# Kernel tuning notes

Measured on AMD Instinct MI355X. Metric: run time of the kernel, lower is better.

## Reference

```python
import jax, jax.numpy as jnp
import numpy as np

BATCH, N_STEPS, STATE_DIM = 8192, 128, 16
HIDDEN = 50
IN0 = STATE_DIM + 1  # features + prev_delta


def _lstm_cell(x, h, c, w_ih, w_hh, b):
    # PyTorch gate order: i, f, g, o
    gates = x @ w_ih.T + h @ w_hh.T + b  # (B, 4H)
    i, f, g, o = jnp.split(gates, 4, axis=-1)
    c_new = jax.nn.sigmoid(f) * c + jax.nn.sigmoid(i) * jnp.tanh(g)
    h_new = jax.nn.sigmoid(o) * jnp.tanh(c_new)
    return h_new, c_new


def setup_inputs() -> dict:
    key = jax.random.key(0)
    ks = jax.random.split(key, 8)
    s = 0.1
    return {
        "features": jax.random.normal(ks[0], (BATCH, N_STEPS, STATE_DIM), dtype=jnp.float32),
        "w_ih0": jax.random.normal(ks[1], (4 * HIDDEN, IN0), dtype=jnp.float32) * s,
        "w_hh0": jax.random.normal(ks[2], (4 * HIDDEN, HIDDEN), dtype=jnp.float32) * s,
        "b_0": jnp.zeros((4 * HIDDEN,), dtype=jnp.float32),  # bias_ih + bias_hh (both init to 0)
        "w_ih1": jax.random.normal(ks[3], (4 * HIDDEN, HIDDEN), dtype=jnp.float32) * s,
        "w_hh1": jax.random.normal(ks[4], (4 * HIDDEN, HIDDEN), dtype=jnp.float32) * s,
        "b_1": jnp.zeros((4 * HIDDEN,), dtype=jnp.float32),
        "w_fc1": jax.random.normal(ks[5], (HIDDEN // 2, HIDDEN), dtype=jnp.float32) * s,
        "b_fc1": jnp.zeros((HIDDEN // 2,), dtype=jnp.float32),
        "w_fc2": jax.random.normal(ks[6], (1, HIDDEN // 2), dtype=jnp.float32) * s,
        "b_fc2": jnp.zeros((1,), dtype=jnp.float32),
    }


def reference(features, w_ih0, w_hh0, b_0, w_ih1, w_hh1, b_1, w_fc1, b_fc1, w_fc2, b_fc2):
    B = features.shape[0]
    feats_t = jnp.swapaxes(features, 0, 1)  # (T, B, state_dim)
    z = jnp.zeros((B, HIDDEN), dtype=features.dtype)
    init = (z, z, z, z, jnp.zeros((B, 1), dtype=features.dtype))

    def step(carry, x_t):
        h0, c0, h1, c1, prev_delta = carry
        x = jnp.concatenate([x_t, prev_delta], axis=-1)  # (B, state_dim+1)
        h0, c0 = _lstm_cell(x, h0, c0, w_ih0, w_hh0, b_0)
        h1, c1 = _lstm_cell(h0, h1, c1, w_ih1, w_hh1, b_1)
        delta = jax.nn.relu(h1 @ w_fc1.T + b_fc1) @ w_fc2.T + b_fc2  # (B, 1)
        return (h0, c0, h1, c1, delta), delta[:, 0]

    _, deltas = jax.lax.scan(step, init, feats_t)  # (T, B)
    return jnp.swapaxes(deltas, 0, 1)  # (B, T)
```

## Files before the change

kernel.cpp:

```cpp
#include <hip/hip_runtime.h>
#include <math.h>

#define BATCH    8192
#define TSTEPS   128
#define SDIM     16
#define HID      50
#define IN0      17
#define BT       16
#define NTHREADS 256

#define RS      160
#define OFF_H0  32
#define OFF_H1  96
#define W0K     96
#define W1K     128
#define WFK     64

typedef _Float16 half_t;
typedef __attribute__((ext_vector_type(8))) _Float16 half8;
typedef __attribute__((ext_vector_type(4))) float    floatx4;

#define MFMA16(a, b, c) __builtin_amdgcn_mfma_f32_16x16x32_f16((a), (b), (c), 0, 0, 0)

__device__ __forceinline__ float sig_u(float x) {
    float e = __expf(-x);
    return __builtin_amdgcn_rcpf(1.0f + e);
}
__device__ __forceinline__ float tanh_u(float x) {
    float e = __expf(-2.0f * x);
    return fmaf(2.0f, __builtin_amdgcn_rcpf(1.0f + e), -1.0f);
}
__device__ __forceinline__ void hsplit(float v, half_t* hp, half_t* lp) {
    half_t h = (half_t)v;
    *hp = h;
    *lp = (half_t)(v - (float)h);
}

__global__ __launch_bounds__(NTHREADS, 2)
void lstm2_uni_kernel(const float* __restrict__ feat,
                      const float* __restrict__ w_ih0,
                      const float* __restrict__ w_hh0,
                      const float* __restrict__ b_0,
                      const float* __restrict__ w_ih1,
                      const float* __restrict__ w_hh1,
                      const float* __restrict__ b_1,
                      const float* __restrict__ w_fc1,
                      const float* __restrict__ b_fc1,
                      const float* __restrict__ w_fc2,
                      const float* __restrict__ b_fc2,
                      float* __restrict__ out)
{
    __shared__ __align__(16) half_t smW[128 * W1K];
    __shared__ __align__(16) half_t Xh[2][BT * RS];
    __shared__ __align__(16) half_t Xl[2][BT * RS];

    const int tid  = threadIdx.x;
    const int lane = tid & 63;
    const int wv   = tid >> 6;
    const int quad = lane >> 4;
    const int col  = lane & 15;
    const int k0q  = quad * 8;
    const int b0   = blockIdx.x * BT;

    auto w0val = [&](int r, int k) -> float {
        if (r >= 200) return 0.0f;
        int j = r >> 2, q = r & 3, orig = q * HID + j;
        if (k < IN0) return w_ih0[orig * IN0 + k];
        if (k < OFF_H0) return 0.0f;
        int u = k - OFF_H0;
        return (u < HID) ? w_hh0[orig * HID + u] : 0.0f;
    };
    auto w1val = [&](int r, int k) -> float {
        if (r >= 200) return 0.0f;
        int j = r >> 2, q = r & 3, orig = q * HID + j;
        if (k < 64) { return (k < HID) ? w_ih1[orig * HID + k] : 0.0f; }
        int u = k - 64;
        return (u < HID) ? w_hh1[orig * HID + u] : 0.0f;
    };

    const int lrow = 64 * (wv & 1) + col;
    half8 a0f[3][4], a1f[4][4];

    #pragma unroll 1
    for (int h = 0; h < 2; ++h) {
        for (int i = tid; i < 128 * W0K; i += NTHREADS) {
            int r = i / W0K, kk = i - r * W0K;
            smW[i] = (half_t)w0val(128 * h + r, kk);
        }
        __syncthreads();
        if ((wv >> 1) == h) {
            #pragma unroll
            for (int kt = 0; kt < 3; ++kt)
                #pragma unroll
                for (int ti = 0; ti < 4; ++ti)
                    a0f[kt][ti] = *(const half8*)(smW + (lrow + 16 * ti) * W0K + 32 * kt + k0q);
        }
        __syncthreads();
    }
    #pragma unroll 1
    for (int h = 0; h < 2; ++h) {
        for (int i = tid; i < 128 * W1K; i += NTHREADS) {
            int r = i >> 7, kk = i & 127;
            smW[i] = (half_t)w1val(128 * h + r, kk);
        }
        __syncthreads();
        if ((wv >> 1) == h) {
            #pragma unroll
            for (int kt = 0; kt < 4; ++kt)
                #pragma unroll
                for (int ti = 0; ti < 4; ++ti)
                    a1f[kt][ti] = *(const half8*)(smW + (lrow + 16 * ti) * W1K + 32 * kt + k0q);
        }
        __syncthreads();
    }
    for (int i = tid; i < 32 * WFK; i += NTHREADS) {
        int r = i >> 6, kk = i & 63;
        smW[i] = (half_t)((r < 25 && kk < HID) ? w_fc1[r * HID + kk] : 0.0f);
    }
    for (int i = tid; i < BT * RS; i += NTHREADS) {
        Xh[0][i] = (half_t)0.0f; Xl[0][i] = (half_t)0.0f;
        Xh[1][i] = (half_t)0.0f; Xl[1][i] = (half_t)0.0f;
    }
    __syncthreads();

    const half8 hz = {0, 0, 0, 0, 0, 0, 0, 0};
    half8 wff[2][2];
    wff[0][0] = hz; wff[0][1] = hz; wff[1][0] = hz; wff[1][1] = hz;
    if (wv == 0) {
        #pragma unroll
        for (int kt = 0; kt < 2; ++kt)
            #pragma unroll
            for (int tf = 0; tf < 2; ++tf)
                wff[kt][tf] = *(const half8*)(smW + (16 * tf + col) * WFK + 32 * kt + k0q);
    }

    const int xs = tid >> 4, xk = tid & 15;
    const size_t fbase = (size_t)(b0 + xs) * (TSTEPS * SDIM) + xk;
    hsplit(feat[fbase], &Xh[0][xs * RS + xk], &Xl[0][xs * RS + xk]);

    floatx4 bias0[4], bias1[4];
    #pragma unroll
    for (int ti = 0; ti < 4; ++ti) {
        floatx4 z = {0.f, 0.f, 0.f, 0.f};
        bias0[ti] = z; bias1[ti] = z;
        int u = 4 * (4 * wv + ti) + quad;
        if (u < HID) {
            bias0[ti][0] = b_0[u];           bias0[ti][1] = b_0[HID + u];
            bias0[ti][2] = b_0[2 * HID + u]; bias0[ti][3] = b_0[3 * HID + u];
            bias1[ti][0] = b_1[u];           bias1[ti][1] = b_1[HID + u];
            bias1[ti][2] = b_1[2 * HID + u]; bias1[ti][3] = b_1[3 * HID + u];
        }
    }
    floatx4 w2r[2], bfr[2];
    { floatx4 z = {0.f, 0.f, 0.f, 0.f}; w2r[0] = z; w2r[1] = z; bfr[0] = z; bfr[1] = z; }
    float bf2 = 0.0f;
    if (wv == 0) {
        bf2 = b_fc2[0];
        #pragma unroll
        for (int tf = 0; tf < 2; ++tf)
            #pragma unroll
            for (int r5 = 0; r5 < 4; ++r5) {
                int r = 16 * tf + quad * 4 + r5;
                if (r < 25) { w2r[tf][r5] = w_fc2[r]; bfr[tf][r5] = b_fc1[r]; }
            }
    }

    float c0s[4] = {0.f, 0.f, 0.f, 0.f};
    float c1s[4] = {0.f, 0.f, 0.f, 0.f};
    half8 nb1h = hz, nb1l = hz, nb2h = hz, nb2l = hz;

    half_t* Xhc = Xh[0]; half_t* Xlc = Xl[0];
    half_t* Xhn = Xh[1]; half_t* Xln = Xl[1];
    __syncthreads();

    for (int t = 0; t < TSTEPS; ++t) {
        float fnext = (t + 1 < TSTEPS) ? feat[fbase + (size_t)(t + 1) * SDIM] : 0.0f;

        floatx4 acc[4];
        #pragma unroll
        for (int ti = 0; ti < 4; ++ti) acc[ti] = bias0[ti];
        {
            half8 bh = *(const half8*)(Xhc + col * RS + k0q);
            half8 bl = *(const half8*)(Xlc + col * RS + k0q);
            #pragma unroll
            for (int ti = 0; ti < 4; ++ti) {
                acc[ti] = MFMA16(a0f[0][ti], bh, acc[ti]);
                acc[ti] = MFMA16(a0f[0][ti], bl, acc[ti]);
            }
        }
        #pragma unroll
        for (int ti = 0; ti < 4; ++ti) {
            acc[ti] = MFMA16(a0f[1][ti], nb1h, acc[ti]);
            acc[ti] = MFMA16(a0f[1][ti], nb1l, acc[ti]);
            acc[ti] = MFMA16(a0f[2][ti], nb2h, acc[ti]);
            acc[ti] = MFMA16(a0f[2][ti], nb2l, acc[ti]);
        }

        #pragma unroll
        for (int ti = 0; ti < 4; ++ti) {
            int u = 4 * (4 * wv + ti) + quad;
            float i_ = sig_u(acc[ti][0]);
            float f_ = sig_u(acc[ti][1]);
            float g_ = tanh_u(acc[ti][2]);
            float o_ = sig_u(acc[ti][3]);
            float c  = f_ * c0s[ti] + i_ * g_;
            c0s[ti]  = c;
            float hv = o_ * tanh_u(c);
            half_t hh, hl; hsplit(hv, &hh, &hl);
            Xhn[col * RS + OFF_H0 + u] = hh;
            Xln[col * RS + OFF_H0 + u] = hl;
        }
        __syncthreads();

        floatx4 acc1[4];
        #pragma unroll
        for (int ti = 0; ti < 4; ++ti) acc1[ti] = bias1[ti];
        nb1h = *(const half8*)(Xhn + col * RS + OFF_H0 + k0q);
        nb1l = *(const half8*)(Xln + col * RS + OFF_H0 + k0q);
        #pragma unroll
        for (int ti = 0; ti < 4; ++ti) {
            acc1[ti] = MFMA16(a1f[0][ti], nb1h, acc1[ti]);
            acc1[ti] = MFMA16(a1f[0][ti], nb1l, acc1[ti]);
        }
        nb2h = *(const half8*)(Xhn + col * RS + OFF_H0 + 32 + k0q);
        nb2l = *(const half8*)(Xln + col * RS + OFF_H0 + 32 + k0q);
        #pragma unroll
        for (int ti = 0; ti < 4; ++ti) {
            acc1[ti] = MFMA16(a1f[1][ti], nb2h, acc1[ti]);
            acc1[ti] = MFMA16(a1f[1][ti], nb2l, acc1[ti]);
        }
        #pragma unroll
        for (int kt = 2; kt < 4; ++kt) {
            half8 bh = *(const half8*)(Xhc + col * RS + OFF_H1 + 32 * (kt - 2) + k0q);
            half8 bl = *(const half8*)(Xlc + col * RS + OFF_H1 + 32 * (kt - 2) + k0q);
            #pragma unroll
            for (int ti = 0; ti < 4; ++ti) {
                acc1[ti] = MFMA16(a1f[kt][ti], bh, acc1[ti]);
                acc1[ti] = MFMA16(a1f[kt][ti], bl, acc1[ti]);
            }
        }

        #pragma unroll
        for (int ti = 0; ti < 4; ++ti) {
            int u = 4 * (4 * wv + ti) + quad;
            float i_ = sig_u(acc1[ti][0]);
            float f_ = sig_u(acc1[ti][1]);
            float g_ = tanh_u(acc1[ti][2]);
            float o_ = sig_u(acc1[ti][3]);
            float c  = f_ * c1s[ti] + i_ * g_;
            c1s[ti]  = c;
            float hv = o_ * tanh_u(c);
            half_t hh, hl; hsplit(hv, &hh, &hl);
            Xhn[col * RS + OFF_H1 + u] = hh;
            Xln[col * RS + OFF_H1 + u] = hl;
        }
        __syncthreads();

        if (wv == 0) {
            floatx4 accf[2]; accf[0] = bfr[0]; accf[1] = bfr[1];
            #pragma unroll
            for (int kt = 0; kt < 2; ++kt) {
                half8 bh = *(const half8*)(Xhn + col * RS + OFF_H1 + 32 * kt + k0q);
                half8 bl = *(const half8*)(Xln + col * RS + OFF_H1 + 32 * kt + k0q);
                #pragma unroll
                for (int tf = 0; tf < 2; ++tf) {
                    accf[tf] = MFMA16(wff[kt][tf], bh, accf[tf]);
                    accf[tf] = MFMA16(wff[kt][tf], bl, accf[tf]);
                }
            }
            float p = 0.0f;
            #pragma unroll
            for (int tf = 0; tf < 2; ++tf)
                #pragma unroll
                for (int r5 = 0; r5 < 4; ++r5)
                    p += w2r[tf][r5] * fmaxf(accf[tf][r5], 0.0f);
            p += __shfl_xor(p, 16);
            p += __shfl_xor(p, 32);
            float d = p + bf2;
            if (lane < 16) {
                out[(size_t)(b0 + lane) * TSTEPS + t] = d;
                hsplit(d, &Xhn[lane * RS + 16], &Xln[lane * RS + 16]);
            }
        }
        if (t + 1 < TSTEPS)
            hsplit(fnext, &Xhn[xs * RS + xk], &Xln[xs * RS + xk]);
        __syncthreads();

        half_t* tp;
        tp = Xhc; Xhc = Xhn; Xhn = tp;
        tp = Xlc; Xlc = Xln; Xln = tp;
    }
}

extern "C" void kernel_launch(void* const* d_in, const int* in_sizes, int n_in,
                              void* d_out, int out_size, void* d_ws, size_t ws_size,
                              hipStream_t stream) {
    const float* feat  = (const float*)d_in[0];
    const float* w_ih0 = (const float*)d_in[1];
    const float* w_hh0 = (const float*)d_in[2];
    const float* b_0   = (const float*)d_in[3];
    const float* w_ih1 = (const float*)d_in[4];
    const float* w_hh1 = (const float*)d_in[5];
    const float* b_1   = (const float*)d_in[6];
    const float* w_fc1 = (const float*)d_in[7];
    const float* b_fc1 = (const float*)d_in[8];
    const float* w_fc2 = (const float*)d_in[9];
    const float* b_fc2 = (const float*)d_in[10];
    float* out = (float*)d_out;

    dim3 grid(BATCH / BT);
    dim3 block(NTHREADS);
    hipLaunchKernelGGL(lstm2_uni_kernel, grid, block, 0, stream,
                       feat, w_ih0, w_hh0, b_0, w_ih1, w_hh1, b_1,
                       w_fc1, b_fc1, w_fc2, b_fc2, out);
}
```

Before: 484.8 us.

## Split gate tiles over eight waves and compute FC head redundantly per wave

Doubles the block to eight waves, with each wave owning two gate tiles instead of four, and skips the empty tiles on the last waves. Biases are folded into the weight matrices through constant-one input columns. Every wave now computes the FC head redundantly and keeps the previous delta in registers, which removes the third barrier per timestep and the single-wave head bottleneck. The cost is more redundant MFMA work and lower per-wave MFMA density, and occupancy may be limited by register pressure at 512 threads.

```diff
diff --git a/kernel.cpp b/kernel.cpp
--- a/kernel.cpp
+++ b/kernel.cpp
@@ -7,7 +7,7 @@
 #define HID      50
 #define IN0      17
 #define BT       16
-#define NTHREADS 256
+#define NTHREADS 512
 
 #define RS      160
 #define OFF_H0  32
@@ -36,21 +36,21 @@
     *lp = (half_t)(v - (float)h);
 }
 
-__global__ __launch_bounds__(NTHREADS, 2)
-void lstm2_uni_kernel(const float* __restrict__ feat,
-                      const float* __restrict__ w_ih0,
-                      const float* __restrict__ w_hh0,
-                      const float* __restrict__ b_0,
-                      const float* __restrict__ w_ih1,
-                      const float* __restrict__ w_hh1,
-                      const float* __restrict__ b_1,
-                      const float* __restrict__ w_fc1,
-                      const float* __restrict__ b_fc1,
-                      const float* __restrict__ w_fc2,
-                      const float* __restrict__ b_fc2,
-                      float* __restrict__ out)
+__global__ __launch_bounds__(NTHREADS, 4)
+void lstm2_w8_kernel(const float* __restrict__ feat,
+                     const float* __restrict__ w_ih0,
+                     const float* __restrict__ w_hh0,
+                     const float* __restrict__ b_0,
+                     const float* __restrict__ w_ih1,
+                     const float* __restrict__ w_hh1,
+                     const float* __restrict__ b_1,
+                     const float* __restrict__ w_fc1,
+                     const float* __restrict__ b_fc1,
+                     const float* __restrict__ w_fc2,
+                     const float* __restrict__ b_fc2,
+                     float* __restrict__ out)
 {
-    __shared__ __align__(16) half_t smW[128 * W1K];
+    __shared__ __align__(16) half_t smW[64 * W1K];
     __shared__ __align__(16) half_t Xh[2][BT * RS];
     __shared__ __align__(16) half_t Xl[2][BT * RS];
 
@@ -61,11 +61,13 @@
     const int col  = lane & 15;
     const int k0q  = quad * 8;
     const int b0   = blockIdx.x * BT;
+    const int tcnt = (wv < 6) ? 2 : (wv == 6 ? 1 : 0);
 
     auto w0val = [&](int r, int k) -> float {
         if (r >= 200) return 0.0f;
         int j = r >> 2, q = r & 3, orig = q * HID + j;
-        if (k < IN0) return w_ih0[orig * IN0 + k];
+        if (k < IN0)  return w_ih0[orig * IN0 + k];
+        if (k == IN0) return b_0[orig];
         if (k < OFF_H0) return 0.0f;
         int u = k - OFF_H0;
         return (u < HID) ? w_hh0[orig * HID + u] : 0.0f;
@@ -73,218 +75,223 @@
     auto w1val = [&](int r, int k) -> float {
         if (r >= 200) return 0.0f;
         int j = r >> 2, q = r & 3, orig = q * HID + j;
-        if (k < 64) { return (k < HID) ? w_ih1[orig * HID + k] : 0.0f; }
+        if (k < 64) {
+            if (k < HID)  return w_ih1[orig * HID + k];
+            if (k == HID) return b_1[orig];
+            return 0.0f;
+        }
         int u = k - 64;
         return (u < HID) ? w_hh1[orig * HID + u] : 0.0f;
     };
 
-    const int lrow = 64 * (wv & 1) + col;
-    half8 a0f[3][4], a1f[4][4];
-
+    half8 a0f[3][2], a1f[4][2];
+    const int lbase = 32 * (wv & 1) + col;
     #pragma unroll 1
-    for (int h = 0; h < 2; ++h) {
-        for (int i = tid; i < 128 * W0K; i += NTHREADS) {
-            int r = i / W0K, kk = i - r * W0K;
-            smW[i] = (half_t)w0val(128 * h + r, kk);
-        }
-        __syncthreads();
-        if ((wv >> 1) == h) {
+    for (int c = 0; c < 4; ++c) {
+        for (int i = tid; i < 64 * W0K; i += NTHREADS) {
+            int r = i / W0K, k = i - r * W0K;
+            smW[i] = (half_t)w0val(64 * c + r, k);
+        }
+        __syncthreads();
+        if ((wv >> 1) == c) {
             #pragma unroll
             for (int kt = 0; kt < 3; ++kt)
                 #pragma unroll
-                for (int ti = 0; ti < 4; ++ti)
-                    a0f[kt][ti] = *(const half8*)(smW + (lrow + 16 * ti) * W0K + 32 * kt + k0q);
+                for (int ti = 0; ti < 2; ++ti)
+                    a0f[kt][ti] = *(const half8*)(smW + (lbase + 16 * ti) * W0K + 32 * kt + k0q);
         }
         __syncthreads();
     }
     #pragma unroll 1
-    for (int h = 0; h < 2; ++h) {
-        for (int i = tid; i < 128 * W1K; i += NTHREADS) {
-            int r = i >> 7, kk = i & 127;
-            smW[i] = (half_t)w1val(128 * h + r, kk);
-        }
-        __syncthreads();
-        if ((wv >> 1) == h) {
+    for (int c = 0; c < 4; ++c) {
+        for (int i = tid; i < 64 * W1K; i += NTHREADS) {
+            int r = i >> 7, k = i & 127;
+            smW[i] = (half_t)w1val(64 * c + r, k);
+        }
+        __syncthreads();
+        if ((wv >> 1) == c) {
             #pragma unroll
             for (int kt = 0; kt < 4; ++kt)
                 #pragma unroll
-                for (int ti = 0; ti < 4; ++ti)
-                    a1f[kt][ti] = *(const half8*)(smW + (lrow + 16 * ti) * W1K + 32 * kt + k0q);
+                for (int ti = 0; ti < 2; ++ti)
+                    a1f[kt][ti] = *(const half8*)(smW + (lbase + 16 * ti) * W1K + 32 * kt + k0q);
         }
         __syncthreads();
     }
     for (int i = tid; i < 32 * WFK; i += NTHREADS) {
-        int r = i >> 6, kk = i & 63;
-        smW[i] = (half_t)((r < 25 && kk < HID) ? w_fc1[r * HID + kk] : 0.0f);
-    }
+        int r = i >> 6, k = i & 63;
+        float v = 0.0f;
+        if (r < 25) { if (k < HID) v = w_fc1[r * HID + k]; else if (k == HID) v = b_fc1[r]; }
+        smW[i] = (half_t)v;
+    }
+    __syncthreads();
+    half8 wff[2][2];
+    #pragma unroll
+    for (int kt = 0; kt < 2; ++kt)
+        #pragma unroll
+        for (int tf = 0; tf < 2; ++tf)
+            wff[kt][tf] = *(const half8*)(smW + (16 * tf + col) * WFK + 32 * kt + k0q);
+
     for (int i = tid; i < BT * RS; i += NTHREADS) {
         Xh[0][i] = (half_t)0.0f; Xl[0][i] = (half_t)0.0f;
         Xh[1][i] = (half_t)0.0f; Xl[1][i] = (half_t)0.0f;
     }
     __syncthreads();
-
-    const half8 hz = {0, 0, 0, 0, 0, 0, 0, 0};
-    half8 wff[2][2];
-    wff[0][0] = hz; wff[0][1] = hz; wff[1][0] = hz; wff[1][1] = hz;
-    if (wv == 0) {
-        #pragma unroll
-        for (int kt = 0; kt < 2; ++kt)
-            #pragma unroll
-            for (int tf = 0; tf < 2; ++tf)
-                wff[kt][tf] = *(const half8*)(smW + (16 * tf + col) * WFK + 32 * kt + k0q);
-    }
-
-    const int xs = tid >> 4, xk = tid & 15;
-    const size_t fbase = (size_t)(b0 + xs) * (TSTEPS * SDIM) + xk;
-    hsplit(feat[fbase], &Xh[0][xs * RS + xk], &Xl[0][xs * RS + xk]);
-
-    floatx4 bias0[4], bias1[4];
+    if (tid < BT) {
+        Xh[0][tid * RS + OFF_H0 + HID] = (half_t)1.0f;
+        Xh[1][tid * RS + OFF_H0 + HID] = (half_t)1.0f;
+        Xh[0][tid * RS + OFF_H1 + HID] = (half_t)1.0f;
+        Xh[1][tid * RS + OFF_H1 + HID] = (half_t)1.0f;
+    }
+    const bool stager = (tid < BT * SDIM);
+    const int  xs = tid >> 4, xk = tid & 15;
+    const size_t fbase = (size_t)(b0 + (stager ? xs : 0)) * (TSTEPS * SDIM) + xk;
+    if (stager) hsplit(feat[fbase], &Xh[0][xs * RS + xk], &Xl[0][xs * RS + xk]);
+
+    floatx4 w2r[2];
+    { floatx4 z = {0.f, 0.f, 0.f, 0.f}; w2r[0] = z; w2r[1] = z; }
     #pragma unroll
-    for (int ti = 0; ti < 4; ++ti) {
-        floatx4 z = {0.f, 0.f, 0.f, 0.f};
-        bias0[ti] = z; bias1[ti] = z;
-        int u = 4 * (4 * wv + ti) + quad;
-        if (u < HID) {
-            bias0[ti][0] = b_0[u];           bias0[ti][1] = b_0[HID + u];
-            bias0[ti][2] = b_0[2 * HID + u]; bias0[ti][3] = b_0[3 * HID + u];
-            bias1[ti][0] = b_1[u];           bias1[ti][1] = b_1[HID + u];
-            bias1[ti][2] = b_1[2 * HID + u]; bias1[ti][3] = b_1[3 * HID + u];
-        }
-    }
-    floatx4 w2r[2], bfr[2];
-    { floatx4 z = {0.f, 0.f, 0.f, 0.f}; w2r[0] = z; w2r[1] = z; bfr[0] = z; bfr[1] = z; }
-    float bf2 = 0.0f;
-    if (wv == 0) {
-        bf2 = b_fc2[0];
-        #pragma unroll
-        for (int tf = 0; tf < 2; ++tf)
-            #pragma unroll
-            for (int r5 = 0; r5 < 4; ++r5) {
-                int r = 16 * tf + quad * 4 + r5;
-                if (r < 25) { w2r[tf][r5] = w_fc2[r]; bfr[tf][r5] = b_fc1[r]; }
-            }
-    }
-
-    float c0s[4] = {0.f, 0.f, 0.f, 0.f};
-    float c1s[4] = {0.f, 0.f, 0.f, 0.f};
-    half8 nb1h = hz, nb1l = hz, nb2h = hz, nb2l = hz;
+    for (int tf = 0; tf < 2; ++tf)
+        #pragma unroll
+        for (int r5 = 0; r5 < 4; ++r5) {
+            int r = 16 * tf + 4 * quad + r5;
+            if (r < 25) w2r[tf][r5] = w_fc2[r];
+        }
+    const float bf2 = b_fc2[0];
+
+    const half8   hz = {0, 0, 0, 0, 0, 0, 0, 0};
+    const floatx4 fz = {0.f, 0.f, 0.f, 0.f};
+    float c0s[2] = {0.f, 0.f};
+    float c1s[2] = {0.f, 0.f};
+    half_t dh = (half_t)0.0f, dl = (half_t)0.0f;
 
     half_t* Xhc = Xh[0]; half_t* Xlc = Xl[0];
     half_t* Xhn = Xh[1]; half_t* Xln = Xl[1];
     __syncthreads();
 
     for (int t = 0; t < TSTEPS; ++t) {
-        float fnext = (t + 1 < TSTEPS) ? feat[fbase + (size_t)(t + 1) * SDIM] : 0.0f;
-
-        floatx4 acc[4];
-        #pragma unroll
-        for (int ti = 0; ti < 4; ++ti) acc[ti] = bias0[ti];
-        {
-            half8 bh = *(const half8*)(Xhc + col * RS + k0q);
-            half8 bl = *(const half8*)(Xlc + col * RS + k0q);
-            #pragma unroll
-            for (int ti = 0; ti < 4; ++ti) {
-                acc[ti] = MFMA16(a0f[0][ti], bh, acc[ti]);
-                acc[ti] = MFMA16(a0f[0][ti], bl, acc[ti]);
-            }
-        }
-        #pragma unroll
-        for (int ti = 0; ti < 4; ++ti) {
-            acc[ti] = MFMA16(a0f[1][ti], nb1h, acc[ti]);
-            acc[ti] = MFMA16(a0f[1][ti], nb1l, acc[ti]);
-            acc[ti] = MFMA16(a0f[2][ti], nb2h, acc[ti]);
-            acc[ti] = MFMA16(a0f[2][ti], nb2l, acc[ti]);
-        }
-
-        #pragma unroll
-        for (int ti = 0; ti < 4; ++ti) {
-            int u = 4 * (4 * wv + ti) + quad;
-            float i_ = sig_u(acc[ti][0]);
-            float f_ = sig_u(acc[ti][1]);
-            float g_ = tanh_u(acc[ti][2]);
-            float o_ = sig_u(acc[ti][3]);
-            float c  = f_ * c0s[ti] + i_ * g_;
-            c0s[ti]  = c;
-            float hv = o_ * tanh_u(c);
-            half_t hh, hl; hsplit(hv, &hh, &hl);
-            Xhn[col * RS + OFF_H0 + u] = hh;
-            Xln[col * RS + OFF_H0 + u] = hl;
-        }
-        __syncthreads();
-
-        floatx4 acc1[4];
-        #pragma unroll
-        for (int ti = 0; ti < 4; ++ti) acc1[ti] = bias1[ti];
-        nb1h = *(const half8*)(Xhn + col * RS + OFF_H0 + k0q);
-        nb1l = *(const half8*)(Xln + col * RS + OFF_H0 + k0q);
-        #pragma unroll
-        for (int ti = 0; ti < 4; ++ti) {
-            acc1[ti] = MFMA16(a1f[0][ti], nb1h, acc1[ti]);
-            acc1[ti] = MFMA16(a1f[0][ti], nb1l, acc1[ti]);
-        }
-        nb2h = *(const half8*)(Xhn + col * RS + OFF_H0 + 32 + k0q);
-        nb2l = *(const half8*)(Xln + col * RS + OFF_H0 + 32 + k0q);
-        #pragma unroll
-        for (int ti = 0; ti < 4; ++ti) {
-            acc1[ti] = MFMA16(a1f[1][ti], nb2h, acc1[ti]);
-            acc1[ti] = MFMA16(a1f[1][ti], nb2l, acc1[ti]);
-        }
-        #pragma unroll
-        for (int kt = 2; kt < 4; ++kt) {
-            half8 bh = *(const half8*)(Xhc + col * RS + OFF_H1 + 32 * (kt - 2) + k0q);
-            half8 bl = *(const half8*)(Xlc + col * RS + OFF_H1 + 32 * (kt - 2) + k0q);
-            #pragma unroll
-            for (int ti = 0; ti < 4; ++ti) {
-                acc1[ti] = MFMA16(a1f[kt][ti], bh, acc1[ti]);
-                acc1[ti] = MFMA16(a1f[kt][ti], bl, acc1[ti]);
-            }
-        }
-
-        #pragma unroll
-        for (int ti = 0; ti < 4; ++ti) {
-            int u = 4 * (4 * wv + ti) + quad;
-            float i_ = sig_u(acc1[ti][0]);
-            float f_ = sig_u(acc1[ti][1]);
-            float g_ = tanh_u(acc1[ti][2]);
-            float o_ = sig_u(acc1[ti][3]);
-            float c  = f_ * c1s[ti] + i_ * g_;
-            c1s[ti]  = c;
-            float hv = o_ * tanh_u(c);
-            half_t hh, hl; hsplit(hv, &hh, &hl);
-            Xhn[col * RS + OFF_H1 + u] = hh;
-            Xln[col * RS + OFF_H1 + u] = hl;
-        }
-        __syncthreads();
-
-        if (wv == 0) {
-            floatx4 accf[2]; accf[0] = bfr[0]; accf[1] = bfr[1];
+        float fnext = 0.0f;
+        if (stager && (t + 1 < TSTEPS)) fnext = feat[fbase + (size_t)(t + 1) * SDIM];
+
+        floatx4 acc[2]; acc[0] = fz; acc[1] = fz;
+        if (tcnt > 0) {
+            half8 bh0, bl0;
+            if (quad < 2) {
+                bh0 = *(const half8*)(Xhc + col * RS + k0q);
+                bl0 = *(const half8*)(Xlc + col * RS + k0q);
+            } else {
+                bh0 = hz; bl0 = hz;
+                if (quad == 2) { bh0[0] = dh; bh0[1] = (half_t)1.0f; bl0[0] = dl; }
+            }
+            #pragma unroll
+            for (int ti = 0; ti < 2; ++ti)
+                if (ti < tcnt) {
+                    acc[ti] = MFMA16(a0f[0][ti], bh0, acc[ti]);
+                    acc[ti] = MFMA16(a0f[0][ti], bl0, acc[ti]);
+                }
+            #pragma unroll
+            for (int kt = 1; kt < 3; ++kt) {
+                half8 bh = *(const half8*)(Xhc + col * RS + OFF_H0 + 32 * (kt - 1) + k0q);
+                half8 bl = *(const half8*)(Xlc + col * RS + OFF_H0 + 32 * (kt - 1) + k0q);
+                #pragma unroll
+                for (int ti = 0; ti < 2; ++ti)
+                    if (ti < tcnt) {
+                        acc[ti] = MFMA16(a0f[kt][ti], bh, acc[ti]);
+                        acc[ti] = MFMA16(a0f[kt][ti], bl, acc[ti]);
+                    }
+            }
+        }
+
+        #pragma unroll
+        for (int ti = 0; ti < 2; ++ti)
+            if (ti < tcnt) {
+                int u = 8 * wv + 4 * ti + quad;
+                float i_ = sig_u(acc[ti][0]);
+                float f_ = sig_u(acc[ti][1]);
+                float g_ = tanh_u(acc[ti][2]);
+                float o_ = sig_u(acc[ti][3]);
+                float c  = f_ * c0s[ti] + i_ * g_;
+                c0s[ti]  = c;
+                float hv = o_ * tanh_u(c);
+                if (u < HID) {
+                    half_t hh, hl; hsplit(hv, &hh, &hl);
+                    Xhn[col * RS + OFF_H0 + u] = hh;
+                    Xln[col * RS + OFF_H0 + u] = hl;
+                }
+            }
+        __syncthreads();
+
+        if (stager && (t + 1 < TSTEPS))
+            hsplit(fnext, &Xhn[xs * RS + xk], &Xln[xs * RS + xk]);
+
+        floatx4 acc1[2]; acc1[0] = fz; acc1[1] = fz;
+        if (tcnt > 0) {
             #pragma unroll
             for (int kt = 0; kt < 2; ++kt) {
-                half8 bh = *(const half8*)(Xhn + col * RS + OFF_H1 + 32 * kt + k0q);
-                half8 bl = *(const half8*)(Xln + col * RS + OFF_H1 + 32 * kt + k0q);
-                #pragma unroll
-                for (int tf = 0; tf < 2; ++tf) {
-                    accf[tf] = MFMA16(wff[kt][tf], bh, accf[tf]);
-                    accf[tf] = MFMA16(wff[kt][tf], bl, accf[tf]);
+                half8 bh = *(const half8*)(Xhn + col * RS + OFF_H0 + 32 * kt + k0q);
+                half8 bl = *(const half8*)(Xln + col * RS + OFF_H0 + 32 * kt + k0q);
+                #pragma unroll
+                for (int ti = 0; ti < 2; ++ti)
+                    if (ti < tcnt) {
+                        acc1[ti] = MFMA16(a1f[kt][ti], bh, acc1[ti]);
+                        acc1[ti] = MFMA16(a1f[kt][ti], bl, acc1[ti]);
+                    }
+            }
+            #pragma unroll
+            for (int kt = 2; kt < 4; ++kt) {
+                half8 bh = *(const half8*)(Xhc + col * RS + OFF_H1 + 32 * (kt - 2) + k0q);
+                half8 bl = *(const half8*)(Xlc + col * RS + OFF_H1 + 32 * (kt - 2) + k0q);
+                #pragma unroll
+                for (int ti = 0; ti < 2; ++ti)
+                    if (ti < tcnt) {
+                        acc1[ti] = MFMA16(a1f[kt][ti], bh, acc1[ti]);
+                        acc1[ti] = MFMA16(a1f[kt][ti], bl, acc1[ti]);
+                    }
+            }
+        }
+
+        #pragma unroll
+        for (int ti = 0; ti < 2; ++ti)
+            if (ti < tcnt) {
+                int u = 8 * wv + 4 * ti + quad;
+                float i_ = sig_u(acc1[ti][0]);
+                float f_ = sig_u(acc1[ti][1]);
+                float g_ = tanh_u(acc1[ti][2]);
+                float o_ = sig_u(acc1[ti][3]);
+                float c  = f_ * c1s[ti] + i_ * g_;
+                c1s[ti]  = c;
+                float hv = o_ * tanh_u(c);
+                if (u < HID) {
+                    half_t hh, hl; hsplit(hv, &hh, &hl);
+                    Xhn[col * RS + OFF_H1 + u] = hh;
+                    Xln[col * RS + OFF_H1 + u] = hl;
                 }
             }
-            float p = 0.0f;
-            #pragma unroll
-            for (int tf = 0; tf < 2; ++tf)
-                #pragma unroll
-                for (int r5 = 0; r5 < 4; ++r5)
-                    p += w2r[tf][r5] * fmaxf(accf[tf][r5], 0.0f);
-            p += __shfl_xor(p, 16);
-            p += __shfl_xor(p, 32);
-            float d = p + bf2;
-            if (lane < 16) {
-                out[(size_t)(b0 + lane) * TSTEPS + t] = d;
-                hsplit(d, &Xhn[lane * RS + 16], &Xln[lane * RS + 16]);
-            }
-        }
-        if (t + 1 < TSTEPS)
-            hsplit(fnext, &Xhn[xs * RS + xk], &Xln[xs * RS + xk]);
-        __syncthreads();
+        __syncthreads();
+
+        floatx4 accf[2]; accf[0] = fz; accf[1] = fz;
+        #pragma unroll
+        for (int kt = 0; kt < 2; ++kt) {
+            half8 bh = *(const half8*)(Xhn + col * RS + OFF_H1 + 32 * kt + k0q);
+            half8 bl = *(const half8*)(Xln + col * RS + OFF_H1 + 32 * kt + k0q);
+            #pragma unroll
+            for (int tf = 0; tf < 2; ++tf) {
+                accf[tf] = MFMA16(wff[kt][tf], bh, accf[tf]);
+                accf[tf] = MFMA16(wff[kt][tf], bl, accf[tf]);
+            }
+        }
+        float p = 0.0f;
+        #pragma unroll
+        for (int tf = 0; tf < 2; ++tf)
+            #pragma unroll
+            for (int r5 = 0; r5 < 4; ++r5)
+                p += w2r[tf][r5] * fmaxf(accf[tf][r5], 0.0f);
+        p += __shfl_xor(p, 16);
+        p += __shfl_xor(p, 32);
+        float d = p + bf2;
+        if (wv == 0 && lane < 16)
+            out[(size_t)(b0 + lane) * TSTEPS + t] = d;
+        hsplit(d, &dh, &dl);
 
         half_t* tp;
         tp = Xhc; Xhc = Xhn; Xhn = tp;
@@ -310,7 +317,7 @@
 
     dim3 grid(BATCH / BT);
     dim3 block(NTHREADS);
-    hipLaunchKernelGGL(lstm2_uni_kernel, grid, block, 0, stream,
+    hipLaunchKernelGGL(lstm2_w8_kernel, grid, block, 0, stream,
                        feat, w_ih0, w_hh0, b_0, w_ih1, w_hh1, b_1,
                        w_fc1, b_fc1, w_fc2, b_fc2, out);
 }
```

Result: no change. 478.0 us (-1.4%).
